# Performance work log

Hardware: AMD Instinct MI355X
Metric: run time of the kernel (lower is better)

Reference implementation:

```python
import jax, jax.numpy as jnp
import numpy as np

B, NG, GS, D, L, NDL = 16, 50, 20, 256, 3, 2
N = NG * GS  # 1000


def setup_inputs() -> dict:
    key = jax.random.key(0)
    ks = jax.random.split(key, 8)
    amino_embd = jax.random.normal(ks[0], (B, NG, GS, D), dtype=jnp.float32)
    c = (jax.random.uniform(ks[1], (B, N, N)) < 0.02).astype(jnp.float32)
    prot_contacts = jnp.clip(c + jnp.transpose(c, (0, 2, 1)), 0.0, 1.0)
    # small init for bilinear W (original: random_uniform ~ +/-0.05) keeps exp() stable
    W_list = 0.01 * jax.random.normal(ks[2], (L, D, D), dtype=jnp.float32)
    dense_W = jax.random.normal(ks[3], (L, NDL, D, D), dtype=jnp.float32) / np.sqrt(D)
    dense_b = jnp.zeros((L, NDL, D), dtype=jnp.float32)
    final_W = jax.random.normal(ks[4], (D, D), dtype=jnp.float32) / np.sqrt(D)
    final_b = jnp.zeros((D,), dtype=jnp.float32)
    return {"amino_embd": amino_embd, "prot_contacts": prot_contacts,
            "W_list": W_list, "dense_W": dense_W, "dense_b": dense_b,
            "final_W": final_W, "final_b": final_b}


def reference(amino_embd, prot_contacts, W_list, dense_W, dense_b, final_W, final_b):
    dt = amino_embd.dtype
    eye = jnp.eye(N, dtype=dt)
    A = prot_contacts + eye  # contact map with self loops, [B,N,N]
    x = amino_embd.reshape(B, N, D)
    for l in range(L):
        x0 = x
        # bilinear non-local scores: [B,N,N]
        scores = jnp.einsum('bid,de,bje->bij', x0, W_list[l], x0)
        s = jnp.exp(scores) + jnp.asarray(1e-5, dt) * eye
        s = s * A                                   # mask by contacts + self loop
        s = s / jnp.sum(s, axis=-1, keepdims=True)  # row-normalize
        x = jnp.einsum('bij,bjd->bid', s, x0)       # aggregate
        for dl in range(NDL):
            x = jax.nn.relu(x @ dense_W[l, dl] + dense_b[l, dl])
        x = x + x0  # skip connection
    x = x @ final_W + final_b
    return x.reshape(B, NG, GS, D)
```

## Files before the change

### kernel.cpp

```cpp
#include <hip/hip_runtime.h>

#define BB 16
#define NN 1000
#define DD 256
#define LL 3
#define MAXNZ 256
#define MROWS (BB * NN)
#define SPLIT_SCALE 2048.0f
#define INV_SPLIT 4.8828125e-4f

typedef _Float16 f16x8 __attribute__((ext_vector_type(8)));
typedef _Float16 f16x2 __attribute__((ext_vector_type(2)));
typedef float f32x4 __attribute__((ext_vector_type(4)));

union H8 { f16x8 v; f16x2 p[4]; _Float16 h[8]; int4 i4; };

#if defined(__has_builtin)
#if __has_builtin(__builtin_amdgcn_fdot2)
#define HAS_FDOT2 1
#endif
#endif

__device__ __forceinline__ float dot2f(f16x2 a, f16x2 b, float c) {
#ifdef HAS_FDOT2
    return __builtin_amdgcn_fdot2(a, b, c, false);
#else
    return fmaf((float)a[0], (float)b[0], fmaf((float)a[1], (float)b[1], c));
#endif
}

__global__ __launch_bounds__(256) void convert_w(
    const float* __restrict__ W_list, const float* __restrict__ dense_W,
    const float* __restrict__ final_W,
    _Float16* __restrict__ wt_hi, _Float16* __restrict__ wt_lo)
{
    __shared__ float T[64][68];
    int blk = blockIdx.x;
    int mat = blk >> 4;
    int tile = blk & 15;
    int tk = (tile >> 2) * 64, tn = (tile & 3) * 64;
    const float* src = (mat < 3) ? (W_list + (size_t)mat * 65536)
                     : (mat < 9) ? (dense_W + (size_t)(mat - 3) * 65536)
                                 : final_W;
    int t = threadIdx.x;
    {
        int k = t >> 2, nc = (t & 3) * 16;
        const float* sp = src + (size_t)(tk + k) * 256 + tn + nc;
        *(float4*)&T[k][nc + 0]  = *(const float4*)(sp + 0);
        *(float4*)&T[k][nc + 4]  = *(const float4*)(sp + 4);
        *(float4*)&T[k][nc + 8]  = *(const float4*)(sp + 8);
        *(float4*)&T[k][nc + 12] = *(const float4*)(sp + 12);
    }
    __syncthreads();
    int n = t >> 2, kc = (t & 3) * 16;
    H8 hh0, hh1, ll0, ll1;
    #pragma unroll
    for (int i = 0; i < 16; ++i) {
        float x = T[kc + i][n];
        _Float16 hi = (_Float16)x;
        _Float16 lo = (_Float16)((x - (float)hi) * SPLIT_SCALE);
        if (i < 8) { hh0.h[i] = hi; ll0.h[i] = lo; }
        else       { hh1.h[i - 8] = hi; ll1.h[i - 8] = lo; }
    }
    size_t o = (size_t)mat * 65536 + (size_t)(tn + n) * 256 + tk + kc;
    *(int4*)(wt_hi + o)     = hh0.i4;
    *(int4*)(wt_hi + o + 8) = hh1.i4;
    *(int4*)(wt_lo + o)     = ll0.i4;
    *(int4*)(wt_lo + o + 8) = ll1.i4;
}

__global__ __launch_bounds__(256) void convert_x(
    const float* __restrict__ in, _Float16* __restrict__ hi,
    _Float16* __restrict__ lo)
{
    size_t gid = (size_t)blockIdx.x * 256 + threadIdx.x;
    const float* p = in + gid * 8;
    float4 a = *(const float4*)p;
    float4 b = *(const float4*)(p + 4);
    float xs[8] = {a.x, a.y, a.z, a.w, b.x, b.y, b.z, b.w};
    H8 hh, ll;
    #pragma unroll
    for (int i = 0; i < 8; ++i) {
        _Float16 h = (_Float16)xs[i];
        hh.h[i] = h;
        ll.h[i] = (_Float16)((xs[i] - (float)h) * SPLIT_SCALE);
    }
    *(int4*)(hi + gid * 8) = hh.i4;
    *(int4*)(lo + gid * 8) = ll.i4;
}

__global__ __launch_bounds__(256) void build_sparse(
    const float* __restrict__ contacts,
    int* __restrict__ idx, int* __restrict__ cnt, float* __restrict__ adiag)
{
    int wave = (int)((blockIdx.x * blockDim.x + threadIdx.x) >> 6);
    int lane = threadIdx.x & 63;
    if (wave >= MROWS) return;
    int b = wave / NN;
    int i = wave - b * NN;
    const float* row = contacts + (size_t)b * NN * NN + (size_t)i * NN;
    int* out = idx + (size_t)wave * MAXNZ;
    int count = 0;
    for (int j0 = 0; j0 < NN; j0 += 64) {
        int j = j0 + lane;
        float v = (j < NN) ? row[j] : 0.0f;
        bool p = (v != 0.0f) && (j != i);
        unsigned long long bal = __ballot(p);
        if (p) {
            int pre = __popcll(bal & ((1ull << lane) - 1ull));
            out[count + pre] = j;
        }
        count += __popcll(bal);
    }
    if (lane == 0) {
        cnt[wave] = count;
        adiag[wave] = row[i] + 1.0f;
    }
}

__global__ __launch_bounds__(256) void sparse_agg(
    const _Float16* __restrict__ yhi,
    const _Float16* __restrict__ xhi, const _Float16* __restrict__ xlo,
    const int* __restrict__ idx, const int* __restrict__ cnt,
    const float* __restrict__ adiag,
    _Float16* __restrict__ ohi, _Float16* __restrict__ olo)
{
    int bid = blockIdx.x;
    int xcd = bid & 7;
    int chunk = bid >> 3;
    int row = xcd * 2000 + chunk * 4 + (int)(threadIdx.x >> 6);
    row = __builtin_amdgcn_readfirstlane(row);
    int lane = threadIdx.x & 63;
    int g = lane >> 4, s = lane & 15;
    int b = row / NN;

    const _Float16* yp = yhi + (size_t)row * DD + s * 8;
    H8 yh0, yh1;
    yh0.i4 = *(const int4*)yp;
    yh1.i4 = *(const int4*)(yp + 128);

    const _Float16* xph = xhi + (size_t)row * DD + s * 8;
    const _Float16* xpl = xlo + (size_t)row * DD + s * 8;
    H8 xih0, xih1, xil0, xil1;
    xih0.i4 = *(const int4*)xph;       xih1.i4 = *(const int4*)(xph + 128);
    xil0.i4 = *(const int4*)xpl;       xil1.i4 = *(const int4*)(xpl + 128);
    float xi[16];
    #pragma unroll
    for (int u = 0; u < 8; ++u) {
        xi[u]     = fmaf((float)xil0.h[u], INV_SPLIT, (float)xih0.h[u]);
        xi[8 + u] = fmaf((float)xil1.h[u], INV_SPLIT, (float)xih1.h[u]);
    }
    const _Float16* xb = xhi + (size_t)b * NN * DD;

    float p = 0.0f;
    #pragma unroll
    for (int u = 0; u < 8; ++u) {
        p = fmaf((float)yh0.h[u], xi[u], p);
        p = fmaf((float)yh1.h[u], xi[8 + u], p);
    }
    p += __shfl_xor(p, 1); p += __shfl_xor(p, 2);
    p += __shfl_xor(p, 4); p += __shfl_xor(p, 8);
    float wd = (g == 0) ? (__expf(p) + 1e-5f) * adiag[row] : 0.0f;
    float denom = wd;
    float acc[16];
    #pragma unroll
    for (int u = 0; u < 16; ++u) acc[u] = wd * xi[u];

    const int c = cnt[row];
    const int* ip = idx + (size_t)row * MAXNZ;
    const int iters = (c + 3) >> 2;

    int j0 = (g < c) ? ip[g] : 0;
    int j1 = (4 + g < c) ? ip[4 + g] : 0;
    bool vok = g < c;
    H8 v0, v1;
    {
        const _Float16* xp = xb + (size_t)j0 * DD + s * 8;
        v0.i4 = *(const int4*)xp;
        v1.i4 = *(const int4*)(xp + 128);
    }

    for (int t = 0; t < iters; ++t) {
        int k2 = (t + 2) * 4 + g;
        int j2 = (k2 < c) ? ip[k2] : 0;
        H8 n0, n1;
        const _Float16* np = xb + (size_t)j1 * DD + s * 8;
        n0.i4 = *(const int4*)np;
        n1.i4 = *(const int4*)(np + 128);

        float q = 0.0f;
        #pragma unroll
        for (int i = 0; i < 4; ++i) q = dot2f(yh0.p[i], v0.p[i], q);
        #pragma unroll
        for (int i = 0; i < 4; ++i) q = dot2f(yh1.p[i], v1.p[i], q);
        q += __shfl_xor(q, 1); q += __shfl_xor(q, 2);
        q += __shfl_xor(q, 4); q += __shfl_xor(q, 8);
        float w = vok ? __expf(q) : 0.0f;
        denom += w;
        #pragma unroll
        for (int u = 0; u < 8; ++u) {
            acc[u]     = fmaf(w, (float)v0.h[u], acc[u]);
            acc[8 + u] = fmaf(w, (float)v1.h[u], acc[8 + u]);
        }

        v0 = n0; v1 = n1;
        j1 = j2;
        vok = (t + 1) * 4 + g < c;
    }

#define XG(x) x += __shfl_xor(x, 16); x += __shfl_xor(x, 32);
    XG(denom);
    #pragma unroll
    for (int u = 0; u < 16; ++u) { XG(acc[u]) }
#undef XG

    float inv = 1.0f / denom;
    int half = (g & 1) * 8;
    H8 st;
    #pragma unroll
    for (int i = 0; i < 8; ++i) {
        float x = acc[half + i] * inv;
        _Float16 h = (_Float16)x;
        st.h[i] = (g & 2) ? (_Float16)((x - (float)h) * SPLIT_SCALE) : h;
    }
    _Float16* dst = ((g & 2) ? olo : ohi) + (size_t)row * DD + (g & 1) * 128 + s * 8;
    *(int4*)dst = st.i4;
}

__global__ __launch_bounds__(256, 4) void gemm16(
    const _Float16* __restrict__ Ahi, const _Float16* __restrict__ Alo,
    const _Float16* __restrict__ Bhi, const _Float16* __restrict__ Blo,
    const float* __restrict__ bias,
    const _Float16* __restrict__ Shi, const _Float16* __restrict__ Slo,
    _Float16* __restrict__ Chi, _Float16* __restrict__ Clo,
    float* __restrict__ Cf32, int relu)
{
    __shared__ __align__(16) char smem[32768];
    char* Ah = smem;
    char* Al = smem + 8192;
    char* Bh = smem + 16384;
    char* Bl = smem + 24576;

    int tid = threadIdx.x;
    int mBase = blockIdx.y * 64;
    int nBase = blockIdx.x * 64;

    int r = tid >> 2;
    int kc = (tid & 3) * 16;
    const _Float16* gAh = Ahi + (size_t)(mBase + r) * 256 + kc;
    const _Float16* gAl = Alo + (size_t)(mBase + r) * 256 + kc;
    const _Float16* gBh = Bhi + (size_t)(nBase + r) * 256 + kc;
    const _Float16* gBl = Blo + (size_t)(nBase + r) * 256 + kc;
    int sbase = r * 128 + kc * 2;
    int swz = (r & 7) << 4;

    int l = tid & 63, wv = tid >> 6;
    int wm = (wv & 1) * 32, wn = (wv >> 1) * 32;
    int lr = l & 15, lk = l >> 4;

    f32x4 acc0[2][2] = {};
    f32x4 acc1[2][2] = {};

    for (int kb = 0; kb < 256; kb += 64) {
        int4 a0 = *(const int4*)(gAh + kb);
        int4 a1 = *(const int4*)(gAh + kb + 8);
        int4 a2 = *(const int4*)(gAl + kb);
        int4 a3 = *(const int4*)(gAl + kb + 8);
        int4 b0 = *(const int4*)(gBh + kb);
        int4 b1 = *(const int4*)(gBh + kb + 8);
        int4 b2 = *(const int4*)(gBl + kb);
        int4 b3 = *(const int4*)(gBl + kb + 8);
        __syncthreads();
        *(int4*)(Ah + ((sbase +  0) ^ swz)) = a0;
        *(int4*)(Ah + ((sbase + 16) ^ swz)) = a1;
        *(int4*)(Al + ((sbase +  0) ^ swz)) = a2;
        *(int4*)(Al + ((sbase + 16) ^ swz)) = a3;
        *(int4*)(Bh + ((sbase +  0) ^ swz)) = b0;
        *(int4*)(Bh + ((sbase + 16) ^ swz)) = b1;
        *(int4*)(Bl + ((sbase +  0) ^ swz)) = b2;
        *(int4*)(Bl + ((sbase + 16) ^ swz)) = b3;
        __syncthreads();

        #pragma unroll
        for (int kk = 0; kk < 2; ++kk) {
            int kby = kk * 64 + lk * 16;
            f16x8 fah[2], fal[2], fbh[2], fbl[2];
            #pragma unroll
            for (int mt = 0; mt < 2; ++mt) {
                int ml = wm + mt * 16 + lr;
                int off = (ml * 128 + kby) ^ ((ml & 7) << 4);
                fah[mt] = *(const f16x8*)(Ah + off);
                fal[mt] = *(const f16x8*)(Al + off);
            }
            #pragma unroll
            for (int nt = 0; nt < 2; ++nt) {
                int nl = wn + nt * 16 + lr;
                int off = (nl * 128 + kby) ^ ((nl & 7) << 4);
                fbh[nt] = *(const f16x8*)(Bh + off);
                fbl[nt] = *(const f16x8*)(Bl + off);
            }
            #pragma unroll
            for (int mt = 0; mt < 2; ++mt)
                #pragma unroll
                for (int nt = 0; nt < 2; ++nt) {
                    acc0[mt][nt] = __builtin_amdgcn_mfma_f32_16x16x32_f16(
                        fah[mt], fbh[nt], acc0[mt][nt], 0, 0, 0);
                    acc1[mt][nt] = __builtin_amdgcn_mfma_f32_16x16x32_f16(
                        fah[mt], fbl[nt], acc1[mt][nt], 0, 0, 0);
                    acc1[mt][nt] = __builtin_amdgcn_mfma_f32_16x16x32_f16(
                        fal[mt], fbh[nt], acc1[mt][nt], 0, 0, 0);
                }
        }
    }

    #pragma unroll
    for (int mt = 0; mt < 2; ++mt) {
        #pragma unroll
        for (int nt = 0; nt < 2; ++nt) {
            int n = nBase + wn + nt * 16 + lr;
            float bv = bias ? bias[n] : 0.0f;
            #pragma unroll
            for (int q = 0; q < 4; ++q) {
                int m = mBase + wm + mt * 16 + lk * 4 + q;
                size_t o = (size_t)m * 256 + n;
                float v = acc0[mt][nt][q] + acc1[mt][nt][q] * INV_SPLIT + bv;
                if (relu) v = fmaxf(v, 0.0f);
                if (Shi) v += (float)Shi[o] + (float)Slo[o] * INV_SPLIT;
                if (Cf32) {
                    Cf32[o] = v;
                } else {
                    _Float16 hh = (_Float16)v;
                    Chi[o] = hh;
                    Clo[o] = (_Float16)((v - (float)hh) * SPLIT_SCALE);
                }
            }
        }
    }
}

extern "C" void kernel_launch(void* const* d_in, const int* in_sizes, int n_in,
                              void* d_out, int out_size, void* d_ws, size_t ws_size,
                              hipStream_t stream)
{
    const float* x_in     = (const float*)d_in[0];
    const float* contacts = (const float*)d_in[1];
    const float* W_list   = (const float*)d_in[2];
    const float* dense_W  = (const float*)d_in[3];
    const float* dense_b  = (const float*)d_in[4];
    const float* final_W  = (const float*)d_in[5];
    const float* final_b  = (const float*)d_in[6];
    float* out = (float*)d_out;

    char* ws = (char*)d_ws;
    const size_t PL = (size_t)MROWS * DD;
    _Float16* pl[8];
    for (int i = 0; i < 8; ++i) pl[i] = (_Float16*)ws + (size_t)i * PL;
    char* p8 = ws + 8 * PL * sizeof(_Float16);
    int*   idx   = (int*)p8;
    int*   cnt   = (int*)(p8 + (size_t)MROWS * MAXNZ * sizeof(int));
    float* adiag = (float*)((char*)cnt + (size_t)MROWS * sizeof(int));
    _Float16* wt_hi = (_Float16*)((char*)adiag + (size_t)MROWS * sizeof(float));
    _Float16* wt_lo = wt_hi + (size_t)10 * 65536;

    convert_w<<<160, 256, 0, stream>>>(W_list, dense_W, final_W, wt_hi, wt_lo);
    convert_x<<<MROWS * DD / (256 * 8), 256, 0, stream>>>(x_in, pl[0], pl[1]);
    build_sparse<<<MROWS / 4, 256, 0, stream>>>(contacts, idx, cnt, adiag);

    dim3 gg(4, MROWS / 64);
    int cur = 0;
    for (int l = 0; l < LL; ++l) {
        int oth = 1 - cur;
        _Float16 *x0h = pl[2 * cur], *x0l = pl[2 * cur + 1];
        _Float16 *yh  = pl[2 * oth], *yl  = pl[2 * oth + 1];
        _Float16 *xah = pl[4], *xal = pl[5];
        _Float16 *xbh = pl[6], *xbl = pl[7];
        gemm16<<<gg, 256, 0, stream>>>(x0h, x0l,
                                       wt_hi + (size_t)l * 65536,
                                       wt_lo + (size_t)l * 65536,
                                       nullptr, nullptr, nullptr,
                                       yh, yl, nullptr, 0);
        sparse_agg<<<MROWS / 4, 256, 0, stream>>>(yh, x0h, x0l, idx, cnt, adiag,
                                                  xah, xal);
        gemm16<<<gg, 256, 0, stream>>>(xah, xal,
                                       wt_hi + (size_t)(3 + l * 2) * 65536,
                                       wt_lo + (size_t)(3 + l * 2) * 65536,
                                       dense_b + (size_t)(l * 2 + 0) * 256,
                                       nullptr, nullptr,
                                       xbh, xbl, nullptr, 1);
        gemm16<<<gg, 256, 0, stream>>>(xbh, xbl,
                                       wt_hi + (size_t)(4 + l * 2) * 65536,
                                       wt_lo + (size_t)(4 + l * 2) * 65536,
                                       dense_b + (size_t)(l * 2 + 1) * 256,
                                       x0h, x0l,
                                       yh, yl, nullptr, 1);
        cur = oth;
    }
    gemm16<<<gg, 256, 0, stream>>>(pl[2 * cur], pl[2 * cur + 1],
                                   wt_hi + (size_t)9 * 65536,
                                   wt_lo + (size_t)9 * 65536,
                                   final_b, nullptr, nullptr,
                                   nullptr, nullptr, out, 0);
}
```

Before: 308.9 us.

## Merge setup kernels, deepen sparse_agg prefetch, register-prefetch GEMM tiles

Folds the three setup kernels (weight conversion, input split, sparse index build) into one launch that picks its role from the block index, removing two launch gaps. sparse_agg now prefetches neighbour rows two iterations ahead instead of one, so more gather latency is hidden. gemm16 loads the next K-tile from global memory into registers while MFMAs run on the current tile, and its launch-bounds occupancy hint drops from 4 to 3 to make room for the extra registers. The deeper prefetch and register staging raise register pressure, which may lower occupancy.

```diff
diff --git a/kernel.cpp b/kernel.cpp
--- a/kernel.cpp
+++ b/kernel.cpp
@@ -29,92 +29,88 @@
 #endif
 }
 
-__global__ __launch_bounds__(256) void convert_w(
+__global__ __launch_bounds__(256) void setup_all(
     const float* __restrict__ W_list, const float* __restrict__ dense_W,
     const float* __restrict__ final_W,
-    _Float16* __restrict__ wt_hi, _Float16* __restrict__ wt_lo)
-{
-    __shared__ float T[64][68];
-    int blk = blockIdx.x;
-    int mat = blk >> 4;
-    int tile = blk & 15;
-    int tk = (tile >> 2) * 64, tn = (tile & 3) * 64;
-    const float* src = (mat < 3) ? (W_list + (size_t)mat * 65536)
-                     : (mat < 9) ? (dense_W + (size_t)(mat - 3) * 65536)
-                                 : final_W;
-    int t = threadIdx.x;
-    {
-        int k = t >> 2, nc = (t & 3) * 16;
-        const float* sp = src + (size_t)(tk + k) * 256 + tn + nc;
-        *(float4*)&T[k][nc + 0]  = *(const float4*)(sp + 0);
-        *(float4*)&T[k][nc + 4]  = *(const float4*)(sp + 4);
-        *(float4*)&T[k][nc + 8]  = *(const float4*)(sp + 8);
-        *(float4*)&T[k][nc + 12] = *(const float4*)(sp + 12);
-    }
-    __syncthreads();
-    int n = t >> 2, kc = (t & 3) * 16;
-    H8 hh0, hh1, ll0, ll1;
-    #pragma unroll
-    for (int i = 0; i < 16; ++i) {
-        float x = T[kc + i][n];
-        _Float16 hi = (_Float16)x;
-        _Float16 lo = (_Float16)((x - (float)hi) * SPLIT_SCALE);
-        if (i < 8) { hh0.h[i] = hi; ll0.h[i] = lo; }
-        else       { hh1.h[i - 8] = hi; ll1.h[i - 8] = lo; }
-    }
-    size_t o = (size_t)mat * 65536 + (size_t)(tn + n) * 256 + tk + kc;
-    *(int4*)(wt_hi + o)     = hh0.i4;
-    *(int4*)(wt_hi + o + 8) = hh1.i4;
-    *(int4*)(wt_lo + o)     = ll0.i4;
-    *(int4*)(wt_lo + o + 8) = ll1.i4;
-}
-
-__global__ __launch_bounds__(256) void convert_x(
-    const float* __restrict__ in, _Float16* __restrict__ hi,
-    _Float16* __restrict__ lo)
-{
-    size_t gid = (size_t)blockIdx.x * 256 + threadIdx.x;
-    const float* p = in + gid * 8;
-    float4 a = *(const float4*)p;
-    float4 b = *(const float4*)(p + 4);
-    float xs[8] = {a.x, a.y, a.z, a.w, b.x, b.y, b.z, b.w};
-    H8 hh, ll;
-    #pragma unroll
-    for (int i = 0; i < 8; ++i) {
-        _Float16 h = (_Float16)xs[i];
-        hh.h[i] = h;
-        ll.h[i] = (_Float16)((xs[i] - (float)h) * SPLIT_SCALE);
-    }
-    *(int4*)(hi + gid * 8) = hh.i4;
-    *(int4*)(lo + gid * 8) = ll.i4;
-}
-
-__global__ __launch_bounds__(256) void build_sparse(
+    _Float16* __restrict__ wt_hi, _Float16* __restrict__ wt_lo,
+    const float* __restrict__ x_in,
+    _Float16* __restrict__ xh, _Float16* __restrict__ xl,
     const float* __restrict__ contacts,
     int* __restrict__ idx, int* __restrict__ cnt, float* __restrict__ adiag)
 {
-    int wave = (int)((blockIdx.x * blockDim.x + threadIdx.x) >> 6);
-    int lane = threadIdx.x & 63;
-    if (wave >= MROWS) return;
-    int b = wave / NN;
-    int i = wave - b * NN;
-    const float* row = contacts + (size_t)b * NN * NN + (size_t)i * NN;
-    int* out = idx + (size_t)wave * MAXNZ;
-    int count = 0;
-    for (int j0 = 0; j0 < NN; j0 += 64) {
-        int j = j0 + lane;
-        float v = (j < NN) ? row[j] : 0.0f;
-        bool p = (v != 0.0f) && (j != i);
-        unsigned long long bal = __ballot(p);
-        if (p) {
-            int pre = __popcll(bal & ((1ull << lane) - 1ull));
-            out[count + pre] = j;
-        }
-        count += __popcll(bal);
-    }
-    if (lane == 0) {
-        cnt[wave] = count;
-        adiag[wave] = row[i] + 1.0f;
+    __shared__ float T[64][68];
+    int bid = blockIdx.x;
+    int t = threadIdx.x;
+
+    if (bid < 160) {
+        int mat = bid >> 4;
+        int tile = bid & 15;
+        int tk = (tile >> 2) * 64, tn = (tile & 3) * 64;
+        const float* src = (mat < 3) ? (W_list + (size_t)mat * 65536)
+                         : (mat < 9) ? (dense_W + (size_t)(mat - 3) * 65536)
+                                     : final_W;
+        {
+            int k = t >> 2, nc = (t & 3) * 16;
+            const float* sp = src + (size_t)(tk + k) * 256 + tn + nc;
+            *(float4*)&T[k][nc + 0]  = *(const float4*)(sp + 0);
+            *(float4*)&T[k][nc + 4]  = *(const float4*)(sp + 4);
+            *(float4*)&T[k][nc + 8]  = *(const float4*)(sp + 8);
+            *(float4*)&T[k][nc + 12] = *(const float4*)(sp + 12);
+        }
+        __syncthreads();
+        int n = t >> 2, kc = (t & 3) * 16;
+        H8 hh0, hh1, ll0, ll1;
+        #pragma unroll
+        for (int i = 0; i < 16; ++i) {
+            float x = T[kc + i][n];
+            _Float16 hi = (_Float16)x;
+            _Float16 lo = (_Float16)((x - (float)hi) * SPLIT_SCALE);
+            if (i < 8) { hh0.h[i] = hi; ll0.h[i] = lo; }
+            else       { hh1.h[i - 8] = hi; ll1.h[i - 8] = lo; }
+        }
+        size_t o = (size_t)mat * 65536 + (size_t)(tn + n) * 256 + tk + kc;
+        *(int4*)(wt_hi + o)     = hh0.i4;
+        *(int4*)(wt_hi + o + 8) = hh1.i4;
+        *(int4*)(wt_lo + o)     = ll0.i4;
+        *(int4*)(wt_lo + o + 8) = ll1.i4;
+    } else if (bid < 2160) {
+        size_t gid = (size_t)(bid - 160) * 256 + t;
+        const float* p = x_in + gid * 8;
+        float4 a = *(const float4*)p;
+        float4 b = *(const float4*)(p + 4);
+        float xs[8] = {a.x, a.y, a.z, a.w, b.x, b.y, b.z, b.w};
+        H8 hh, ll;
+        #pragma unroll
+        for (int i = 0; i < 8; ++i) {
+            _Float16 h = (_Float16)xs[i];
+            hh.h[i] = h;
+            ll.h[i] = (_Float16)((xs[i] - (float)h) * SPLIT_SCALE);
+        }
+        *(int4*)(xh + gid * 8) = hh.i4;
+        *(int4*)(xl + gid * 8) = ll.i4;
+    } else {
+        int wave = (int)(((size_t)(bid - 2160) * 256 + t) >> 6);
+        int lane = t & 63;
+        int b = wave / NN;
+        int i = wave - b * NN;
+        const float* row = contacts + (size_t)b * NN * NN + (size_t)i * NN;
+        int* out = idx + (size_t)wave * MAXNZ;
+        int count = 0;
+        for (int j0 = 0; j0 < NN; j0 += 64) {
+            int j = j0 + lane;
+            float v = (j < NN) ? row[j] : 0.0f;
+            bool p = (v != 0.0f) && (j != i);
+            unsigned long long bal = __ballot(p);
+            if (p) {
+                int pre = __popcll(bal & ((1ull << lane) - 1ull));
+                out[count + pre] = j;
+            }
+            count += __popcll(bal);
+        }
+        if (lane == 0) {
+            cnt[wave] = count;
+            adiag[wave] = row[i] + 1.0f;
+        }
     }
 }
 
@@ -170,24 +166,29 @@
     const int* ip = idx + (size_t)row * MAXNZ;
     const int iters = (c + 3) >> 2;
 
-    int j0 = (g < c) ? ip[g] : 0;
-    int j1 = (4 + g < c) ? ip[4 + g] : 0;
-    bool vok = g < c;
-    H8 v0, v1;
+    int j2;
+    H8 v0, v1, n0, n1;
     {
-        const _Float16* xp = xb + (size_t)j0 * DD + s * 8;
-        v0.i4 = *(const int4*)xp;
-        v1.i4 = *(const int4*)(xp + 128);
+        int ja = (g < c) ? ip[g] : 0;
+        int jb = (4 + g < c) ? ip[4 + g] : 0;
+        j2 = (8 + g < c) ? ip[8 + g] : 0;
+        const _Float16* p0 = xb + (size_t)ja * DD + s * 8;
+        v0.i4 = *(const int4*)p0;
+        v1.i4 = *(const int4*)(p0 + 128);
+        const _Float16* p1 = xb + (size_t)jb * DD + s * 8;
+        n0.i4 = *(const int4*)p1;
+        n1.i4 = *(const int4*)(p1 + 128);
     }
 
     for (int t = 0; t < iters; ++t) {
-        int k2 = (t + 2) * 4 + g;
-        int j2 = (k2 < c) ? ip[k2] : 0;
-        H8 n0, n1;
-        const _Float16* np = xb + (size_t)j1 * DD + s * 8;
-        n0.i4 = *(const int4*)np;
-        n1.i4 = *(const int4*)(np + 128);
-
+        int k3 = (t + 3) * 4 + g;
+        int j3 = (k3 < c) ? ip[k3] : 0;
+        H8 m0, m1;
+        const _Float16* mp = xb + (size_t)j2 * DD + s * 8;
+        m0.i4 = *(const int4*)mp;
+        m1.i4 = *(const int4*)(mp + 128);
+
+        bool vok = t * 4 + g < c;
         float q = 0.0f;
         #pragma unroll
         for (int i = 0; i < 4; ++i) q = dot2f(yh0.p[i], v0.p[i], q);
@@ -204,8 +205,8 @@
         }
 
         v0 = n0; v1 = n1;
-        j1 = j2;
-        vok = (t + 1) * 4 + g < c;
+        n0 = m0; n1 = m1;
+        j2 = j3;
     }
 
 #define XG(x) x += __shfl_xor(x, 16); x += __shfl_xor(x, 32);
@@ -227,7 +228,7 @@
     *(int4*)dst = st.i4;
 }
 
-__global__ __launch_bounds__(256, 4) void gemm16(
+__global__ __launch_bounds__(256, 3) void gemm16(
     const _Float16* __restrict__ Ahi, const _Float16* __restrict__ Alo,
     const _Float16* __restrict__ Bhi, const _Float16* __restrict__ Blo,
     const float* __restrict__ bias,
@@ -261,25 +262,29 @@
     f32x4 acc0[2][2] = {};
     f32x4 acc1[2][2] = {};
 
+    int4 rA0, rA1, rA2, rA3, rB0, rB1, rB2, rB3;
+#define LOADG(kb) \
+    rA0 = *(const int4*)(gAh + (kb));     rA1 = *(const int4*)(gAh + (kb) + 8); \
+    rA2 = *(const int4*)(gAl + (kb));     rA3 = *(const int4*)(gAl + (kb) + 8); \
+    rB0 = *(const int4*)(gBh + (kb));     rB1 = *(const int4*)(gBh + (kb) + 8); \
+    rB2 = *(const int4*)(gBl + (kb));     rB3 = *(const int4*)(gBl + (kb) + 8);
+
+    LOADG(0)
+
+    #pragma unroll
     for (int kb = 0; kb < 256; kb += 64) {
-        int4 a0 = *(const int4*)(gAh + kb);
-        int4 a1 = *(const int4*)(gAh + kb + 8);
-        int4 a2 = *(const int4*)(gAl + kb);
-        int4 a3 = *(const int4*)(gAl + kb + 8);
-        int4 b0 = *(const int4*)(gBh + kb);
-        int4 b1 = *(const int4*)(gBh + kb + 8);
-        int4 b2 = *(const int4*)(gBl + kb);
-        int4 b3 = *(const int4*)(gBl + kb + 8);
         __syncthreads();
-        *(int4*)(Ah + ((sbase +  0) ^ swz)) = a0;
-        *(int4*)(Ah + ((sbase + 16) ^ swz)) = a1;
-        *(int4*)(Al + ((sbase +  0) ^ swz)) = a2;
-        *(int4*)(Al + ((sbase + 16) ^ swz)) = a3;
-        *(int4*)(Bh + ((sbase +  0) ^ swz)) = b0;
-        *(int4*)(Bh + ((sbase + 16) ^ swz)) = b1;
-        *(int4*)(Bl + ((sbase +  0) ^ swz)) = b2;
-        *(int4*)(Bl + ((sbase + 16) ^ swz)) = b3;
+        *(int4*)(Ah + ((sbase +  0) ^ swz)) = rA0;
+        *(int4*)(Ah + ((sbase + 16) ^ swz)) = rA1;
+        *(int4*)(Al + ((sbase +  0) ^ swz)) = rA2;
+        *(int4*)(Al + ((sbase + 16) ^ swz)) = rA3;
+        *(int4*)(Bh + ((sbase +  0) ^ swz)) = rB0;
+        *(int4*)(Bh + ((sbase + 16) ^ swz)) = rB1;
+        *(int4*)(Bl + ((sbase +  0) ^ swz)) = rB2;
+        *(int4*)(Bl + ((sbase + 16) ^ swz)) = rB3;
         __syncthreads();
+
+        if (kb < 192) { LOADG(kb + 64) }
 
         #pragma unroll
         for (int kk = 0; kk < 2; ++kk) {
@@ -312,6 +317,7 @@
                 }
         }
     }
+#undef LOADG
 
     #pragma unroll
     for (int mt = 0; mt < 2; ++mt) {
@@ -362,9 +368,9 @@
     _Float16* wt_hi = (_Float16*)((char*)adiag + (size_t)MROWS * sizeof(float));
     _Float16* wt_lo = wt_hi + (size_t)10 * 65536;
 
-    convert_w<<<160, 256, 0, stream>>>(W_list, dense_W, final_W, wt_hi, wt_lo);
-    convert_x<<<MROWS * DD / (256 * 8), 256, 0, stream>>>(x_in, pl[0], pl[1]);
-    build_sparse<<<MROWS / 4, 256, 0, stream>>>(contacts, idx, cnt, adiag);
+    setup_all<<<6160, 256, 0, stream>>>(W_list, dense_W, final_W, wt_hi, wt_lo,
+                                        x_in, pl[0], pl[1],
+                                        contacts, idx, cnt, adiag);
 
     dim3 gg(4, MROWS / 64);
     int cur = 0;
```

Result: no change. 303.0 us (-1.9%).
